# Performance work log

Hardware: AMD Instinct MI355X
Metric: run time of the kernel (lower is better)

Reference implementation:

```python
import jax, jax.numpy as jnp
import numpy as np

HIDDEN = 4096
N_HEADS = 32
N_KV_HEADS = 8
HEAD_DIM = HIDDEN // N_HEADS          # 128
GROUP = N_HEADS // N_KV_HEADS         # 4 q-heads per kv-head
Q_SIZE = N_HEADS * HEAD_DIM           # 4096
KV_SIZE = N_KV_HEADS * HEAD_DIM       # 1024
T = 2048


def setup_inputs() -> dict:
    key = jax.random.key(0)
    k1, k2, k3 = jax.random.split(key, 3)
    positions = jnp.arange(T, dtype=jnp.int64) if jax.config.jax_enable_x64 else jnp.arange(T, dtype=jnp.int32)
    hidden_states = jax.random.normal(k1, (T, HIDDEN), dtype=jnp.float32)
    # torch.nn.Linear weights: out = x @ W.T
    w_qkv = jax.random.normal(k2, (Q_SIZE + 2 * KV_SIZE, HIDDEN), dtype=jnp.float32) * 0.02
    w_o = jax.random.normal(k3, (HIDDEN, HIDDEN), dtype=jnp.float32) * 0.02
    return {"positions": positions, "hidden_states": hidden_states, "w_qkv": w_qkv, "w_o": w_o}


def reference(positions, hidden_states, w_qkv, w_o):
    del positions  # rotary is a no-op in the fake module
    t = hidden_states.shape[0]
    scaling = HEAD_DIM ** -0.5

    qkv = hidden_states @ w_qkv.T                              # [T, q+2kv]
    q, k, v = jnp.split(qkv, [Q_SIZE, Q_SIZE + KV_SIZE], axis=-1)
    # GQA mapping: q-head h uses kv-head h // GROUP (contiguous groups)
    q = q.reshape(t, N_KV_HEADS, GROUP, HEAD_DIM)              # [T, Hkv, G, d]
    k = k.reshape(t, N_KV_HEADS, HEAD_DIM)                     # [T, Hkv, d]
    v = v.reshape(t, N_KV_HEADS, HEAD_DIM)

    # Cache starts empty -> token i attends to keys 0..i (causal prefill)
    logits = jnp.einsum('tkgd,skd->kgts', q, k) * scaling      # [Hkv, G, T, T]
    causal = jnp.tril(jnp.ones((t, t), dtype=bool))            # s <= t
    logits = jnp.where(causal, logits, jnp.finfo(logits.dtype).min)
    weights = jax.nn.softmax(logits, axis=-1)
    ctx = jnp.einsum('kgts,skd->tkgd', weights, v)             # [T, Hkv, G, d]
    ctx = ctx.reshape(t, HIDDEN)
    return ctx @ w_o.T
```

## Files before the change

### kernel.cpp

```cpp
#include <hip/hip_runtime.h>

typedef unsigned short u16;
typedef __bf16 bf16x8 __attribute__((ext_vector_type(8)));
typedef float f32x4 __attribute__((ext_vector_type(4)));

__device__ __forceinline__ u16 f2bf(float f) {
  union { float f; unsigned u; } v; v.f = f;
  unsigned r = v.u + 0x7FFFu + ((v.u >> 16) & 1u);
  return (u16)(r >> 16);
}

__device__ __forceinline__ void gload16(const void* g, void* l) {
  __builtin_amdgcn_global_load_lds(
      (const __attribute__((address_space(1))) unsigned int*)g,
      (__attribute__((address_space(3))) unsigned int*)l, 16, 0, 0);
}

__global__ __launch_bounds__(256) void cvt_bf16(const float* __restrict__ in,
                                                u16* __restrict__ out, long n) {
  long i = ((long)blockIdx.x * 256 + threadIdx.x) * 8;
  const long stride = (long)gridDim.x * 2048;
  for (; i < n; i += stride) {
    float4 a = *(const float4*)(in + i);
    float4 b = *(const float4*)(in + i + 4);
    uint4 o;
    o.x = (unsigned)f2bf(a.x) | ((unsigned)f2bf(a.y) << 16);
    o.y = (unsigned)f2bf(a.z) | ((unsigned)f2bf(a.w) << 16);
    o.z = (unsigned)f2bf(b.x) | ((unsigned)f2bf(b.y) << 16);
    o.w = (unsigned)f2bf(b.z) | ((unsigned)f2bf(b.w) << 16);
    *(uint4*)(out + i) = o;
  }
}

template <int BM, int BN, typename OUT>
__global__ __launch_bounds__(512, 2) void gemmT(const u16* __restrict__ A,
                                                const u16* __restrict__ B,
                                                OUT* __restrict__ C,
                                                int M, int N, int K) {
  constexpr int MREP = BM / 32;
  constexpr int NREP = BN / 64;
  constexpr int MPP = MREP / 4;
  constexpr int AI = BM / 64;
  constexpr int BI = BN / 64;
  __shared__ __align__(16) u16 sA[2][BM * 64];
  __shared__ __align__(16) u16 sB[2][BN * 64];

  const int tid = threadIdx.x;
  const int w = tid >> 6, ln = tid & 63;
  const int lr = ln & 15, lg = ln >> 4;
  const int wr = w >> 2, wc = w & 3;

  const int nN = N / BN;
  const int bm = (blockIdx.x / nN) * BM;
  const int bn = (blockIdx.x % nN) * BN;

  const int srow = tid >> 3;
  const int scol = (((tid & 7) * 16) ^ ((srow & 7) << 4)) >> 1;
  const u16* pA = A + (size_t)(bm + srow) * K + scol;
  const u16* pB = B + (size_t)(bn + srow) * K + scol;

  const int mask = (lr & 7) << 4;
  const int pAr = (wr * (BM / 2) + lr) * 128;
  const int pBr = (wc * (BN / 4) + lr) * 128;

  f32x4 acc[MREP][NREP] = {};
  const int nk = K >> 6;

  auto stage = [&](int buf, int t) {
    const int k0 = t << 6;
#pragma unroll
    for (int i = 0; i < AI; ++i)
      gload16(pA + (size_t)i * 64 * K + k0, (char*)sA[buf] + i * 8192 + tid * 16);
#pragma unroll
    for (int i = 0; i < BI; ++i)
      gload16(pB + (size_t)i * 64 * K + k0, (char*)sB[buf] + i * 8192 + tid * 16);
  };

  stage(0, 0);

#pragma unroll 1
  for (int t = 0; t < nk; ++t) {
    const int buf = t & 1;
    const char* lA = (const char*)sA[buf];
    const char* lB = (const char*)sB[buf];

    asm volatile("s_waitcnt vmcnt(0)" ::: "memory");
    __builtin_amdgcn_s_barrier();
    __builtin_amdgcn_sched_barrier(0);

    if (t + 1 < nk) stage(buf ^ 1, t + 1);

    bf16x8 bfr[NREP][2];
#pragma unroll
    for (int nf = 0; nf < NREP; ++nf)
#pragma unroll
      for (int s = 0; s < 2; ++s)
        bfr[nf][s] = *(const bf16x8*)(lB + pBr + nf * 2048 +
                                      ((lg * 16 + s * 64) ^ mask));

#pragma unroll
    for (int p = 0; p < 4; ++p) {
      if (p) __builtin_amdgcn_s_barrier();
      bf16x8 af[MPP][2];
#pragma unroll
      for (int m = 0; m < MPP; ++m)
#pragma unroll
        for (int s = 0; s < 2; ++s)
          af[m][s] = *(const bf16x8*)(lA + pAr + (p * MPP + m) * 2048 +
                                      ((lg * 16 + s * 64) ^ mask));
      asm volatile("s_waitcnt lgkmcnt(0)" ::: "memory");
      __builtin_amdgcn_sched_barrier(0);
      __builtin_amdgcn_s_setprio(1);
#pragma unroll
      for (int s = 0; s < 2; ++s)
#pragma unroll
        for (int m = 0; m < MPP; ++m)
#pragma unroll
          for (int nf = 0; nf < NREP; ++nf)
            acc[p * MPP + m][nf] = __builtin_amdgcn_mfma_f32_16x16x32_bf16(
                af[m][s], bfr[nf][s], acc[p * MPP + m][nf], 0, 0, 0);
      __builtin_amdgcn_s_setprio(0);
    }
  }

#pragma unroll
  for (int m = 0; m < MREP; ++m)
#pragma unroll
    for (int nf = 0; nf < NREP; ++nf)
#pragma unroll
      for (int r = 0; r < 4; ++r) {
        const int row = bm + wr * (BM / 2) + m * 16 + lg * 4 + r;
        const int col = bn + wc * (BN / 4) + nf * 16 + lr;
        const float v = acc[m][nf][r];
        if constexpr (sizeof(OUT) == 2)
          C[(size_t)row * N + col] = (OUT)f2bf(v);
        else
          C[(size_t)row * N + col] = v;
      }
}

__global__ __launch_bounds__(256) void vtrans(const u16* __restrict__ qkv,
                                              u16* __restrict__ vT) {
  __shared__ u16 tile[128][65];
  const int hk = blockIdx.y;
  const int tb = blockIdx.x * 64;
  const int tid = threadIdx.x;
#pragma unroll
  for (int p = 0; p < 4; ++p) {
    const int tr = p * 16 + (tid >> 4);
    const int d0 = (tid & 15) * 8;
    const uint4 x = *(const uint4*)(qkv + (size_t)(tb + tr) * 6144 + 5120 + hk * 128 + d0);
    const u16* xv = (const u16*)&x;
#pragma unroll
    for (int j = 0; j < 8; ++j) tile[d0 + j][tr] = xv[j];
  }
  __syncthreads();
#pragma unroll
  for (int p = 0; p < 4; ++p) {
    const int d = p * 32 + (tid >> 3);
    const int t0 = (tid & 7) * 8;
    u16 v[8];
#pragma unroll
    for (int j = 0; j < 8; ++j) v[j] = tile[d][t0 + j];
    uint4 o;
    unsigned* ov = (unsigned*)&o;
#pragma unroll
    for (int j = 0; j < 4; ++j)
      ov[j] = (unsigned)v[2 * j] | ((unsigned)v[2 * j + 1] << 16);
    *(uint4*)(vT + (size_t)hk * 128 * 2048 + (size_t)d * 2048 + tb + t0) = o;
  }
}

__global__ __launch_bounds__(256) void attn(const u16* __restrict__ qkv,
                                            const u16* __restrict__ vT,
                                            u16* __restrict__ ctx) {
  __shared__ __align__(16) u16 sK[2][64 * 128];
  __shared__ __align__(16) u16 sV[2][128 * 64];
  __shared__ __align__(16) u16 sP[4 * 16 * 64];
  const int tid = threadIdx.x, w = tid >> 6, ln = tid & 63;
  const int lr = ln & 15, lg = ln >> 4;
  const int h = blockIdx.y, hk = h >> 2;
  const int pi = blockIdx.x;

  const float scale = 0.08838834764831845f;
  const float LOG2E = 1.4426950408889634f;
  char* const pw = (char*)sP + w * 2048;

  auto stage = [&](int buf, int kt) {
    const int kvbase = kt * 64;
#pragma unroll
    for (int i = 0; i < 4; ++i) {
      const int off = i * 4096 + tid * 16;
      {
        const int row = off >> 8, cbp = off & 255;
        const int cb = cbp ^ ((row & 7) << 4);
        gload16(qkv + (size_t)(kvbase + row) * 6144 + 4096 + hk * 128 + (cb >> 1),
                (char*)sK + buf * 16384 + off);
      }
      {
        const int row = off >> 7, cbp = off & 127;
        const int cb = cbp ^ ((row & 7) << 4);
        gload16(vT + (size_t)hk * 262144 + (size_t)row * 2048 + kvbase + (cb >> 1),
                (char*)sV + buf * 16384 + off);
      }
    }
  };

#pragma unroll 1
  for (int ph = 0; ph < 2; ++ph) {
    const int qt = ph ? (31 - pi) : pi;
    const int qbase = qt * 64;
    const int nkt = qt + 1;

    bf16x8 qf[4];
    {
      const u16* qrow = qkv + (size_t)(qbase + w * 16 + lr) * 6144 + h * 128 + lg * 8;
#pragma unroll
      for (int kk = 0; kk < 4; ++kk) qf[kk] = *(const bf16x8*)(qrow + kk * 32);
    }

    f32x4 acc_o[8] = {};
    float m_r[4] = {-INFINITY, -INFINITY, -INFINITY, -INFINITY};
    float l_r[4] = {0.f, 0.f, 0.f, 0.f};

    stage(0, 0);

#pragma unroll 1
    for (int kt = 0; kt < nkt; ++kt) {
      const int buf = kt & 1;
      const int kvbase = kt * 64;
      __syncthreads();
      if (kt + 1 < nkt) stage(buf ^ 1, kt + 1);

      char* const kbase = (char*)sK + buf * 16384;
      char* const vbase = (char*)sV + buf * 16384;

      f32x4 sacc[4] = {};
#pragma unroll
      for (int kk = 0; kk < 4; ++kk) {
#pragma unroll
        for (int nf = 0; nf < 4; ++nf) {
          const int row = nf * 16 + lr;
          const int byt = row * 256 + ((kk * 64 + lg * 16) ^ ((row & 7) << 4));
          const bf16x8 kf = *(const bf16x8*)(kbase + byt);
          sacc[nf] = __builtin_amdgcn_mfma_f32_16x16x32_bf16(qf[kk], kf, sacc[nf], 0, 0, 0);
        }
      }

      const bool diag = (kt == qt);
      float p[4][4];
#pragma unroll
      for (int r = 0; r < 4; ++r) {
        const int qrow = qbase + w * 16 + lg * 4 + r;
        float mx = -INFINITY;
#pragma unroll
        for (int nf = 0; nf < 4; ++nf) {
          float v = sacc[nf][r] * scale;
          if (diag && (kvbase + nf * 16 + lr > qrow)) v = -INFINITY;
          p[nf][r] = v;
          mx = fmaxf(mx, v);
        }
        mx = fmaxf(mx, __shfl_xor(mx, 1));
        mx = fmaxf(mx, __shfl_xor(mx, 2));
        mx = fmaxf(mx, __shfl_xor(mx, 4));
        mx = fmaxf(mx, __shfl_xor(mx, 8));
        const float mt = fmaxf(m_r[r], mx);
        const float alpha = exp2f((m_r[r] - mt) * LOG2E);
        m_r[r] = mt;
        float rs = 0.f;
#pragma unroll
        for (int nf = 0; nf < 4; ++nf) {
          const float e = exp2f((p[nf][r] - mt) * LOG2E);
          p[nf][r] = e;
          rs += e;
        }
        rs += __shfl_xor(rs, 1);
        rs += __shfl_xor(rs, 2);
        rs += __shfl_xor(rs, 4);
        rs += __shfl_xor(rs, 8);
        l_r[r] = l_r[r] * alpha + rs;
#pragma unroll
        for (int o = 0; o < 8; ++o) acc_o[o][r] = acc_o[o][r] * alpha;
      }

#pragma unroll
      for (int r = 0; r < 4; ++r) {
        const int row = lg * 4 + r;
#pragma unroll
        for (int nf = 0; nf < 4; ++nf) {
          const int col = nf * 16 + lr;
          const int byt = row * 128 + ((2 * col) ^ ((row & 7) << 4));
          *(u16*)(pw + byt) = f2bf(p[nf][r]);
        }
      }

#pragma unroll
      for (int kk2 = 0; kk2 < 2; ++kk2) {
        const int pbyt = lr * 128 + ((kk2 * 64 + lg * 16) ^ ((lr & 7) << 4));
        const bf16x8 pf = *(const bf16x8*)(pw + pbyt);
#pragma unroll
        for (int o = 0; o < 8; ++o) {
          const int vrow = o * 16 + lr;
          const int vbyt = vrow * 128 + ((kk2 * 64 + lg * 16) ^ ((vrow & 7) << 4));
          const bf16x8 vf = *(const bf16x8*)(vbase + vbyt);
          acc_o[o] = __builtin_amdgcn_mfma_f32_16x16x32_bf16(pf, vf, acc_o[o], 0, 0, 0);
        }
      }
    }

#pragma unroll
    for (int r = 0; r < 4; ++r) {
      const float inv = 1.f / l_r[r];
      const int t = qbase + w * 16 + lg * 4 + r;
#pragma unroll
      for (int o = 0; o < 8; ++o)
        ctx[(size_t)t * 4096 + h * 128 + o * 16 + lr] = f2bf(acc_o[o][r] * inv);
    }
    __syncthreads();
  }
}

extern "C" void kernel_launch(void* const* d_in, const int* in_sizes, int n_in,
                              void* d_out, int out_size, void* d_ws, size_t ws_size,
                              hipStream_t stream) {
  (void)in_sizes; (void)n_in; (void)out_size; (void)ws_size;
  const float* hidden = (const float*)d_in[1];
  const float* w_qkv = (const float*)d_in[2];
  const float* w_o = (const float*)d_in[3];
  float* out = (float*)d_out;
  char* ws = (char*)d_ws;

  u16* xb    = (u16*)(ws + 0);
  u16* wqkvb = (u16*)(ws + 16777216);
  u16* wob   = (u16*)(ws + 67108864);
  u16* qkvb  = (u16*)(ws + 100663296);
  u16* vTb   = (u16*)(ws + 125829120);
  u16* ctxb  = (u16*)(ws + 130023424);

  cvt_bf16<<<4096, 256, 0, stream>>>(hidden, xb, (long)2048 * 4096);
  cvt_bf16<<<8192, 256, 0, stream>>>(w_qkv, wqkvb, (long)6144 * 4096);
  cvt_bf16<<<8192, 256, 0, stream>>>(w_o, wob, (long)4096 * 4096);
  gemmT<256, 192, u16><<<256, 512, 0, stream>>>(xb, wqkvb, qkvb, 2048, 6144, 4096);
  vtrans<<<dim3(32, 8), 256, 0, stream>>>(qkvb, vTb);
  attn<<<dim3(16, 32), 256, 0, stream>>>(qkvb, vTb, ctxb);
  gemmT<128, 256, float><<<256, 512, 0, stream>>>(ctxb, wob, out, 2048, 4096, 4096);
}
```

Before: 380.3 us.

## Double-buffer A fragments in registers and remap block IDs for locality

The GEMM inner loop now preloads two sets of A fragments and issues the next LDS read while MFMAs on the previous set run, using partial lgkmcnt waits in place of full waits and per-phase barriers. Block indices are also permuted in strides of gridDim/8 so that consecutive hardware blocks map to spread-out tiles, which is meant to improve L2/XCD locality. This costs more registers for the extra fragment buffer, and it assumes gridDim is divisible by 8. Removing the intra-iteration barriers changes how waves synchronise.

Result: faster. 353.0 us (-7.2%).

```diff
diff --git a/kernel.cpp b/kernel.cpp
--- a/kernel.cpp
+++ b/kernel.cpp
@@ -50,9 +50,11 @@
   const int lr = ln & 15, lg = ln >> 4;
   const int wr = w >> 2, wc = w & 3;
 
+  int bid = (int)blockIdx.x;
+  bid = (bid & 7) * ((int)gridDim.x >> 3) + (bid >> 3);
   const int nN = N / BN;
-  const int bm = (blockIdx.x / nN) * BM;
-  const int bn = (blockIdx.x % nN) * BN;
+  const int bm = (bid / nN) * BM;
+  const int bn = (bid % nN) * BN;
 
   const int srow = tid >> 3;
   const int scol = (((tid & 7) * 16) ^ ((srow & 7) << 4)) >> 1;
@@ -90,26 +92,15 @@
 
     if (t + 1 < nk) stage(buf ^ 1, t + 1);
 
-    bf16x8 bfr[NREP][2];
-#pragma unroll
-    for (int nf = 0; nf < NREP; ++nf)
-#pragma unroll
-      for (int s = 0; s < 2; ++s)
-        bfr[nf][s] = *(const bf16x8*)(lB + pBr + nf * 2048 +
-                                      ((lg * 16 + s * 64) ^ mask));
-
-#pragma unroll
-    for (int p = 0; p < 4; ++p) {
-      if (p) __builtin_amdgcn_s_barrier();
-      bf16x8 af[MPP][2];
+    auto readA = [&](bf16x8 (&af)[MPP][2], int p) {
 #pragma unroll
       for (int m = 0; m < MPP; ++m)
 #pragma unroll
         for (int s = 0; s < 2; ++s)
           af[m][s] = *(const bf16x8*)(lA + pAr + (p * MPP + m) * 2048 +
                                       ((lg * 16 + s * 64) ^ mask));
-      asm volatile("s_waitcnt lgkmcnt(0)" ::: "memory");
-      __builtin_amdgcn_sched_barrier(0);
+    };
+    auto mfmaP = [&](bf16x8 (&af)[MPP][2], bf16x8 (&bfr)[NREP][2], int p) {
       __builtin_amdgcn_s_setprio(1);
 #pragma unroll
       for (int s = 0; s < 2; ++s)
@@ -120,7 +111,39 @@
             acc[p * MPP + m][nf] = __builtin_amdgcn_mfma_f32_16x16x32_bf16(
                 af[m][s], bfr[nf][s], acc[p * MPP + m][nf], 0, 0, 0);
       __builtin_amdgcn_s_setprio(0);
-    }
+    };
+
+    bf16x8 bfr[NREP][2];
+#pragma unroll
+    for (int nf = 0; nf < NREP; ++nf)
+#pragma unroll
+      for (int s = 0; s < 2; ++s)
+        bfr[nf][s] = *(const bf16x8*)(lB + pBr + nf * 2048 +
+                                      ((lg * 16 + s * 64) ^ mask));
+    bf16x8 a0[MPP][2], a1[MPP][2];
+    readA(a0, 0);
+    readA(a1, 1);
+
+    if constexpr (MPP == 2) asm volatile("s_waitcnt lgkmcnt(4)" ::: "memory");
+    else                    asm volatile("s_waitcnt lgkmcnt(2)" ::: "memory");
+    __builtin_amdgcn_sched_barrier(0);
+    mfmaP(a0, bfr, 0);
+    readA(a0, 2);
+
+    if constexpr (MPP == 2) asm volatile("s_waitcnt lgkmcnt(4)" ::: "memory");
+    else                    asm volatile("s_waitcnt lgkmcnt(2)" ::: "memory");
+    __builtin_amdgcn_sched_barrier(0);
+    mfmaP(a1, bfr, 1);
+    readA(a1, 3);
+
+    if constexpr (MPP == 2) asm volatile("s_waitcnt lgkmcnt(4)" ::: "memory");
+    else                    asm volatile("s_waitcnt lgkmcnt(2)" ::: "memory");
+    __builtin_amdgcn_sched_barrier(0);
+    mfmaP(a0, bfr, 2);
+
+    asm volatile("s_waitcnt lgkmcnt(0)" ::: "memory");
+    __builtin_amdgcn_sched_barrier(0);
+    mfmaP(a1, bfr, 3);
   }
 
 #pragma unroll
```

## Interleave next-tile global loads across MFMA phases and reshape warp grid

Applied to the files above, without the earlier changes.

Replaces the GEMM kernel with a version whose warp layout is parameterized (WM x WN). Each wave now holds 4 M-fragments, and the K=64 step is split into four phases by k-half and m-half. Prefetch of the next tile is spread across those phases in chunks, so global loads interleave with MFMA work instead of being issued in one burst. This cuts per-phase register pressure for fragments, but adds barriers in every phase and changes the LDS read pattern, which risks more synchronization stalls.

New measurement: 363.4 us. 1.05x faster.

```diff
diff --git a/kernel.cpp b/kernel.cpp
--- a/kernel.cpp
+++ b/kernel.cpp
@@ -32,27 +32,28 @@
   }
 }
 
-template <int BM, int BN, typename OUT>
-__global__ __launch_bounds__(512, 2) void gemmT(const u16* __restrict__ A,
+template <int BM, int BN, int WM, typename OUT>
+__global__ __launch_bounds__(512, 2) void gemmP(const u16* __restrict__ A,
                                                 const u16* __restrict__ B,
                                                 OUT* __restrict__ C,
                                                 int M, int N, int K) {
-  constexpr int MREP = BM / 32;
-  constexpr int NREP = BN / 64;
-  constexpr int MPP = MREP / 4;
+  constexpr int WN = 8 / WM;
+  constexpr int MREP = BM / WM / 16;
+  constexpr int NREP = BN / WN / 16;
   constexpr int AI = BM / 64;
   constexpr int BI = BN / 64;
+  static_assert(MREP == 4, "phase split assumes MREP==4");
   __shared__ __align__(16) u16 sA[2][BM * 64];
   __shared__ __align__(16) u16 sB[2][BN * 64];
 
   const int tid = threadIdx.x;
   const int w = tid >> 6, ln = tid & 63;
   const int lr = ln & 15, lg = ln >> 4;
-  const int wr = w >> 2, wc = w & 3;
+  const int wr = w / WN, wc = w % WN;
 
   const int nN = N / BN;
-  const int bm = (blockIdx.x / nN) * BM;
-  const int bn = (blockIdx.x % nN) * BN;
+  const int bm = ((int)blockIdx.x / nN) * BM;
+  const int bn = ((int)blockIdx.x % nN) * BN;
 
   const int srow = tid >> 3;
   const int scol = (((tid & 7) * 16) ^ ((srow & 7) << 4)) >> 1;
@@ -60,13 +61,13 @@
   const u16* pB = B + (size_t)(bn + srow) * K + scol;
 
   const int mask = (lr & 7) << 4;
-  const int pAr = (wr * (BM / 2) + lr) * 128;
-  const int pBr = (wc * (BN / 4) + lr) * 128;
+  const int pAr = (wr * (BM / WM) + lr) * 128;
+  const int pBr = (wc * (BN / WN) + lr) * 128;
 
   f32x4 acc[MREP][NREP] = {};
   const int nk = K >> 6;
 
-  auto stage = [&](int buf, int t) {
+  auto stageAll = [&](int buf, int t) {
     const int k0 = t << 6;
 #pragma unroll
     for (int i = 0; i < AI; ++i)
@@ -75,8 +76,19 @@
     for (int i = 0; i < BI; ++i)
       gload16(pB + (size_t)i * 64 * K + k0, (char*)sB[buf] + i * 8192 + tid * 16);
   };
-
-  stage(0, 0);
+  auto stageChunk = [&](int buf, int t, int p) {
+    const int k0 = t << 6;
+#pragma unroll
+    for (int i = 0; i < AI; ++i)
+      if ((i & 3) == p)
+        gload16(pA + (size_t)i * 64 * K + k0, (char*)sA[buf] + i * 8192 + tid * 16);
+#pragma unroll
+    for (int i = 0; i < BI; ++i)
+      if (((AI + i) & 3) == p)
+        gload16(pB + (size_t)i * 64 * K + k0, (char*)sB[buf] + i * 8192 + tid * 16);
+  };
+
+  stageAll(0, 0);
 
 #pragma unroll 1
   for (int t = 0; t < nk; ++t) {
@@ -88,37 +100,33 @@
     __builtin_amdgcn_s_barrier();
     __builtin_amdgcn_sched_barrier(0);
 
-    if (t + 1 < nk) stage(buf ^ 1, t + 1);
-
-    bf16x8 bfr[NREP][2];
-#pragma unroll
-    for (int nf = 0; nf < NREP; ++nf)
-#pragma unroll
-      for (int s = 0; s < 2; ++s)
-        bfr[nf][s] = *(const bf16x8*)(lB + pBr + nf * 2048 +
-                                      ((lg * 16 + s * 64) ^ mask));
-
+    bf16x8 bfr[NREP];
 #pragma unroll
     for (int p = 0; p < 4; ++p) {
-      if (p) __builtin_amdgcn_s_barrier();
-      bf16x8 af[MPP][2];
-#pragma unroll
-      for (int m = 0; m < MPP; ++m)
-#pragma unroll
-        for (int s = 0; s < 2; ++s)
-          af[m][s] = *(const bf16x8*)(lA + pAr + (p * MPP + m) * 2048 +
-                                      ((lg * 16 + s * 64) ^ mask));
+      const int s = p >> 1, mh = p & 1;
+      if (mh == 0) {
+#pragma unroll
+        for (int nf = 0; nf < NREP; ++nf)
+          bfr[nf] = *(const bf16x8*)(lB + pBr + nf * 2048 +
+                                     ((lg * 16 + s * 64) ^ mask));
+      }
+      bf16x8 af0 = *(const bf16x8*)(lA + pAr + (2 * mh) * 2048 +
+                                    ((lg * 16 + s * 64) ^ mask));
+      bf16x8 af1 = *(const bf16x8*)(lA + pAr + (2 * mh + 1) * 2048 +
+                                    ((lg * 16 + s * 64) ^ mask));
+      if (t + 1 < nk) stageChunk(buf ^ 1, t + 1, p);
+
+      __builtin_amdgcn_s_barrier();
       asm volatile("s_waitcnt lgkmcnt(0)" ::: "memory");
       __builtin_amdgcn_sched_barrier(0);
       __builtin_amdgcn_s_setprio(1);
 #pragma unroll
-      for (int s = 0; s < 2; ++s)
-#pragma unroll
-        for (int m = 0; m < MPP; ++m)
-#pragma unroll
-          for (int nf = 0; nf < NREP; ++nf)
-            acc[p * MPP + m][nf] = __builtin_amdgcn_mfma_f32_16x16x32_bf16(
-                af[m][s], bfr[nf][s], acc[p * MPP + m][nf], 0, 0, 0);
+      for (int nf = 0; nf < NREP; ++nf) {
+        acc[2 * mh][nf] = __builtin_amdgcn_mfma_f32_16x16x32_bf16(
+            af0, bfr[nf], acc[2 * mh][nf], 0, 0, 0);
+        acc[2 * mh + 1][nf] = __builtin_amdgcn_mfma_f32_16x16x32_bf16(
+            af1, bfr[nf], acc[2 * mh + 1][nf], 0, 0, 0);
+      }
       __builtin_amdgcn_s_setprio(0);
     }
   }
@@ -129,8 +137,8 @@
     for (int nf = 0; nf < NREP; ++nf)
 #pragma unroll
       for (int r = 0; r < 4; ++r) {
-        const int row = bm + wr * (BM / 2) + m * 16 + lg * 4 + r;
-        const int col = bn + wc * (BN / 4) + nf * 16 + lr;
+        const int row = bm + wr * (BM / WM) + m * 16 + lg * 4 + r;
+        const int col = bn + wc * (BN / WN) + nf * 16 + lr;
         const float v = acc[m][nf][r];
         if constexpr (sizeof(OUT) == 2)
           C[(size_t)row * N + col] = (OUT)f2bf(v);
@@ -340,8 +348,8 @@
   cvt_bf16<<<4096, 256, 0, stream>>>(hidden, xb, (long)2048 * 4096);
   cvt_bf16<<<8192, 256, 0, stream>>>(w_qkv, wqkvb, (long)6144 * 4096);
   cvt_bf16<<<8192, 256, 0, stream>>>(w_o, wob, (long)4096 * 4096);
-  gemmT<256, 192, u16><<<256, 512, 0, stream>>>(xb, wqkvb, qkvb, 2048, 6144, 4096);
+  gemmP<256, 192, 4, u16><<<256, 512, 0, stream>>>(xb, wqkvb, qkvb, 2048, 6144, 4096);
   vtrans<<<dim3(32, 8), 256, 0, stream>>>(qkvb, vTb);
   attn<<<dim3(16, 32), 256, 0, stream>>>(qkvb, vTb, ctxb);
-  gemmT<128, 256, float><<<256, 512, 0, stream>>>(ctxb, wob, out, 2048, 4096, 4096);
-}
+  gemmP<128, 256, 2, float><<<256, 512, 0, stream>>>(ctxb, wob, out, 2048, 4096, 4096);
+}
```

## Interleave next-tile global loads across m-quarters with fine-grained vmcnt waits

Applied to the files above, without the earlier changes.

Reorders the A-tile rows in shared memory so each m-quarter's rows arrive in separate load batches. The next tile's global-to-LDS loads are now issued in chunks across the four compute quarters instead of all at once. Partial vmcnt waits replace the full drain at the top of each k-step, so compute on early quarters can begin while later rows are still arriving. This adds barriers and more complex wait accounting, and a wrong vmcnt count would risk reading stale data.

After: 334.6 us. 1.14x faster.

```diff
diff --git a/kernel.cpp b/kernel.cpp
--- a/kernel.cpp
+++ b/kernel.cpp
@@ -33,15 +33,18 @@
 }
 
 template <int BM, int BN, typename OUT>
-__global__ __launch_bounds__(512, 2) void gemmT(const u16* __restrict__ A,
+__global__ __launch_bounds__(512, 2) void gemmQ(const u16* __restrict__ A,
                                                 const u16* __restrict__ B,
                                                 OUT* __restrict__ C,
                                                 int M, int N, int K) {
   constexpr int MREP = BM / 32;
   constexpr int NREP = BN / 64;
-  constexpr int MPP = MREP / 4;
+  constexpr int MQ = MREP / 4;
+  constexpr int QS = MQ * 16;
   constexpr int AI = BM / 64;
   constexpr int BI = BN / 64;
+  constexpr int TE = AI + BI;
+  static_assert(MREP % 4 == 0, "need 4 m-quarters");
   __shared__ __align__(16) u16 sA[2][BM * 64];
   __shared__ __align__(16) u16 sB[2][BN * 64];
 
@@ -51,74 +54,91 @@
   const int wr = w >> 2, wc = w & 3;
 
   const int nN = N / BN;
-  const int bm = (blockIdx.x / nN) * BM;
-  const int bn = (blockIdx.x % nN) * BN;
-
-  const int srow = tid >> 3;
-  const int scol = (((tid & 7) * 16) ^ ((srow & 7) << 4)) >> 1;
-  const u16* pA = A + (size_t)(bm + srow) * K + scol;
-  const u16* pB = B + (size_t)(bn + srow) * K + scol;
+  const int bm = ((int)blockIdx.x / nN) * BM;
+  const int bn = ((int)blockIdx.x % nN) * BN;
+
+  const int s_r = tid >> 3;
+  const int scol = (((tid & 7) * 16) ^ ((s_r & 7) << 4)) >> 1;
+  const int gA0 = ((s_r / QS) & 1) * (BM / 2) + (s_r / (2 * QS)) * QS +
+                  (s_r & (QS - 1));
+  const u16* pAb = A + (size_t)(bm + gA0) * K + scol;
+  const u16* pBb = B + (size_t)(bn + s_r) * K + scol;
 
   const int mask = (lr & 7) << 4;
-  const int pAr = (wr * (BM / 2) + lr) * 128;
   const int pBr = (wc * (BN / 4) + lr) * 128;
 
   f32x4 acc[MREP][NREP] = {};
   const int nk = K >> 6;
 
-  auto stage = [&](int buf, int t) {
-    const int k0 = t << 6;
-#pragma unroll
-    for (int i = 0; i < AI; ++i)
-      gload16(pA + (size_t)i * 64 * K + k0, (char*)sA[buf] + i * 8192 + tid * 16);
-#pragma unroll
-    for (int i = 0; i < BI; ++i)
-      gload16(pB + (size_t)i * 64 * K + k0, (char*)sB[buf] + i * 8192 + tid * 16);
+  auto stage1 = [&](int buf, int k0, int j) {
+    if (j < BI)
+      gload16(pBb + (size_t)j * 64 * K + k0, (char*)sB[buf] + j * 8192 + tid * 16);
+    else {
+      const int i = j - BI;
+      gload16(pAb + (size_t)i * 32 * K + k0, (char*)sA[buf] + i * 8192 + tid * 16);
+    }
   };
 
-  stage(0, 0);
+#pragma unroll
+  for (int j = 0; j < TE; ++j) stage1(0, 0, j);
+
+  constexpr int S[4] = {0, 2, 4, TE - AI / 2};
+  constexpr int E[4] = {2, 4, TE - AI / 2, TE};
 
 #pragma unroll 1
   for (int t = 0; t < nk; ++t) {
     const int buf = t & 1;
+    const int k1 = (t + 1) << 6;
+    const bool more = (t + 1 < nk);
     const char* lA = (const char*)sA[buf];
     const char* lB = (const char*)sB[buf];
 
-    asm volatile("s_waitcnt vmcnt(0)" ::: "memory");
-    __builtin_amdgcn_s_barrier();
-    __builtin_amdgcn_sched_barrier(0);
-
-    if (t + 1 < nk) stage(buf ^ 1, t + 1);
-
     bf16x8 bfr[NREP][2];
 #pragma unroll
-    for (int nf = 0; nf < NREP; ++nf)
-#pragma unroll
-      for (int s = 0; s < 2; ++s)
-        bfr[nf][s] = *(const bf16x8*)(lB + pBr + nf * 2048 +
-                                      ((lg * 16 + s * 64) ^ mask));
-
-#pragma unroll
-    for (int p = 0; p < 4; ++p) {
-      if (p) __builtin_amdgcn_s_barrier();
-      bf16x8 af[MPP][2];
-#pragma unroll
-      for (int m = 0; m < MPP; ++m)
+    for (int q = 0; q < 4; ++q) {
+      if (q == 0) {
+        if constexpr (AI == 4) asm volatile("s_waitcnt vmcnt(2)" ::: "memory");
+        else                   asm volatile("s_waitcnt vmcnt(1)" ::: "memory");
+      } else if (q == 2) {
+        if (more) asm volatile("s_waitcnt vmcnt(4)" ::: "memory");
+        else      asm volatile("s_waitcnt vmcnt(0)" ::: "memory");
+      }
+      __builtin_amdgcn_s_barrier();
+      __builtin_amdgcn_sched_barrier(0);
+
+      if (q == 0) {
+#pragma unroll
+        for (int nf = 0; nf < NREP; ++nf)
+#pragma unroll
+          for (int s = 0; s < 2; ++s)
+            bfr[nf][s] = *(const bf16x8*)(lB + pBr + nf * 2048 +
+                                          ((lg * 16 + s * 64) ^ mask));
+      }
+      bf16x8 af[MQ][2];
+#pragma unroll
+      for (int j = 0; j < MQ; ++j)
 #pragma unroll
         for (int s = 0; s < 2; ++s)
-          af[m][s] = *(const bf16x8*)(lA + pAr + (p * MPP + m) * 2048 +
-                                      ((lg * 16 + s * 64) ^ mask));
+          af[j][s] = *(const bf16x8*)(
+              lA + (q * 2 * QS + wr * QS + j * 16 + lr) * 128 +
+              ((lg * 16 + s * 64) ^ mask));
+
+      if (more) {
+#pragma unroll
+        for (int j = S[q]; j < E[q]; ++j) stage1(buf ^ 1, k1, j);
+      }
+
       asm volatile("s_waitcnt lgkmcnt(0)" ::: "memory");
       __builtin_amdgcn_sched_barrier(0);
       __builtin_amdgcn_s_setprio(1);
 #pragma unroll
       for (int s = 0; s < 2; ++s)
 #pragma unroll
-        for (int m = 0; m < MPP; ++m)
+        for (int j = 0; j < MQ; ++j)
 #pragma unroll
           for (int nf = 0; nf < NREP; ++nf)
-            acc[p * MPP + m][nf] = __builtin_amdgcn_mfma_f32_16x16x32_bf16(
-                af[m][s], bfr[nf][s], acc[p * MPP + m][nf], 0, 0, 0);
+            acc[q * MQ + j][nf] = __builtin_amdgcn_mfma_f32_16x16x32_bf16(
+                af[j][s], bfr[nf][s], acc[q * MQ + j][nf], 0, 0, 0);
       __builtin_amdgcn_s_setprio(0);
     }
   }
@@ -340,8 +360,8 @@
   cvt_bf16<<<4096, 256, 0, stream>>>(hidden, xb, (long)2048 * 4096);
   cvt_bf16<<<8192, 256, 0, stream>>>(w_qkv, wqkvb, (long)6144 * 4096);
   cvt_bf16<<<8192, 256, 0, stream>>>(w_o, wob, (long)4096 * 4096);
-  gemmT<256, 192, u16><<<256, 512, 0, stream>>>(xb, wqkvb, qkvb, 2048, 6144, 4096);
+  gemmQ<256, 192, u16><<<256, 512, 0, stream>>>(xb, wqkvb, qkvb, 2048, 6144, 4096);
   vtrans<<<dim3(32, 8), 256, 0, stream>>>(qkvb, vTb);
   attn<<<dim3(16, 32), 256, 0, stream>>>(qkvb, vTb, ctxb);
-  gemmT<128, 256, float><<<256, 512, 0, stream>>>(ctxb, wob, out, 2048, 4096, 4096);
-}
+  gemmQ<128, 256, float><<<256, 512, 0, stream>>>(ctxb, wob, out, 2048, 4096, 4096);
+}
```
